# Performance work log

Measured on AMD Instinct MI355X. Metric: run time of the kernel, lower is better.

Reference implementation:

```python
import jax, jax.numpy as jnp
import numpy as np

N_HEAD_FULL = 16  # config.n_head

def setup_inputs() -> dict:
    key = jax.random.key(0)
    ks = jax.random.split(key, 5)
    B, T, D = 2, 2048, 2048
    s = 0.02
    return {
        "x": jax.random.normal(ks[0], (B, T, D), dtype=jnp.float32),
        "Wq": jax.random.normal(ks[1], (D, D), dtype=jnp.float32) * s,
        "Wk": jax.random.normal(ks[2], (D, D), dtype=jnp.float32) * s,
        "Wv": jax.random.normal(ks[3], (D, D), dtype=jnp.float32) * s,
        "Wo": jax.random.normal(ks[4], (D, D), dtype=jnp.float32) * s,
        "active_dim": 1024,
        "active_kv": 64,
    }

def reference(x, Wq, Wk, Wv, Wo, active_dim, active_kv):
    B, T, D = x.shape
    d = active_dim if active_dim is not None else D
    head_dim_base = D // N_HEAD_FULL          # 128
    kv_dim = active_kv if active_kv is not None else head_dim_base
    n_head = d // head_dim_base               # active heads
    head_dim = d // n_head                    # == head_dim_base

    xs = x[..., :d]                            # [B,T,d]
    # F.linear(x, W[:d,:d]) == x @ W[:d,:d].T
    q = jnp.einsum('btc,dc->btd', xs, Wq[:d, :d])
    k = jnp.einsum('btc,dc->btd', xs, Wk[:d, :d])
    v = jnp.einsum('btc,dc->btd', xs, Wv[:d, :d])

    def split_heads(t):  # [B,T,d] -> [B,h,T,hd]
        return t.reshape(B, T, n_head, head_dim).transpose(0, 2, 1, 3)
    q, k, v = split_heads(q), split_heads(k), split_heads(v)

    if kv_dim < head_dim:
        q, k, v = q[..., :kv_dim], k[..., :kv_dim], v[..., :kv_dim]

    scale = 1.0 / np.sqrt(kv_dim).astype(np.float32)
    attn = jnp.einsum('bhqd,bhkd->bhqk', q, k) * scale  # [B,h,T,T]
    causal = jnp.tril(jnp.ones((T, T), dtype=bool))
    attn = jnp.where(causal, attn, jnp.float32(-jnp.inf))
    attn = jax.nn.softmax(attn, axis=-1)
    out = jnp.einsum('bhqk,bhkd->bhqd', attn, v)        # [B,h,T,kv]

    if kv_dim < head_dim:
        out = jnp.pad(out, ((0, 0), (0, 0), (0, 0), (0, head_dim - kv_dim)))
    out = out.transpose(0, 2, 1, 3).reshape(B, T, d)
    out = jnp.einsum('btc,dc->btd', out, Wo[:d, :d])
    if d < D:
        out = jnp.pad(out, ((0, 0), (0, 0), (0, D - d)))
    return out
```

## Files before the change

kernel.cpp:

```cpp
#include <hip/hip_runtime.h>
#include <hip/hip_bf16.h>

typedef __attribute__((ext_vector_type(8))) short bf16x8;
typedef __attribute__((ext_vector_type(4))) float f32x4;

#define MFMA16(a,b,c) __builtin_amdgcn_mfma_f32_16x16x32_bf16((a),(b),(c),0,0,0)

static __device__ __forceinline__ unsigned short f2bf(float f) {
    unsigned int u = __builtin_bit_cast(unsigned int, f);
    u += 0x7fffu + ((u >> 16) & 1u);
    return (unsigned short)(u >> 16);
}

static __device__ __forceinline__ void g2l16(const unsigned short* g, unsigned short* l) {
    __builtin_amdgcn_global_load_lds(
        (const __attribute__((address_space(1))) unsigned int*)g,
        (__attribute__((address_space(3))) unsigned int*)l,
        16, 0, 0);
}

#define BT     4096
#define DFULL  2048
#define DACT   1024
#define DKV    64
#define NSEL   512
#define TSEQ   2048
#define PADR   72

__global__ __launch_bounds__(256) void prep_kernel(
    const float* __restrict__ x,  const float* __restrict__ Wq,
    const float* __restrict__ Wk, const float* __restrict__ Wv,
    const float* __restrict__ Wo,
    unsigned short* __restrict__ xb,  unsigned short* __restrict__ Wqb,
    unsigned short* __restrict__ Wkb, unsigned short* __restrict__ Wvb,
    unsigned short* __restrict__ Wob, float* __restrict__ out)
{
    const int NA = (BT * DACT) / 8;
    const int NB = (NSEL * DACT) / 8;
    const int NC = (DACT * NSEL) / 8;
    const int ND = (BT * DACT) / 8;
    const int TOT = NA + 3 * NB + NC + ND;
    for (int u = blockIdx.x * blockDim.x + threadIdx.x; u < TOT;
         u += gridDim.x * blockDim.x) {
        if (u < NA) {
            int e = u * 8; int row = e >> 10, col = e & 1023;
            const float* s = x + (size_t)row * DFULL + col;
            f32x4 v0 = *(const f32x4*)s, v1 = *(const f32x4*)(s + 4);
            bf16x8 o;
            #pragma unroll
            for (int j = 0; j < 4; ++j) { o[j] = (short)f2bf(v0[j]); o[4+j] = (short)f2bf(v1[j]); }
            *(bf16x8*)(xb + e) = o;
        } else if (u < NA + 3 * NB) {
            int t = u - NA; int mat = t / NB; int q = t % NB;
            int e = q * 8; int n = e >> 10, c = e & 1023;
            const float* W = (mat == 0) ? Wq : (mat == 1) ? Wk : Wv;
            unsigned short* Wb = (mat == 0) ? Wqb : (mat == 1) ? Wkb : Wvb;
            int wrow = (n >> 6) * 128 + (n & 63);
            const float* s = W + (size_t)wrow * DFULL + c;
            f32x4 v0 = *(const f32x4*)s, v1 = *(const f32x4*)(s + 4);
            bf16x8 o;
            #pragma unroll
            for (int j = 0; j < 4; ++j) { o[j] = (short)f2bf(v0[j]); o[4+j] = (short)f2bf(v1[j]); }
            *(bf16x8*)(Wb + e) = o;
        } else if (u < NA + 3 * NB + NC) {
            int q = u - NA - 3 * NB;
            int e = q * 8; int r = e >> 9, cs = e & 511;
            int col = (cs >> 6) * 128 + (cs & 63);
            const float* s = Wo + (size_t)r * DFULL + col;
            f32x4 v0 = *(const f32x4*)s, v1 = *(const f32x4*)(s + 4);
            bf16x8 o;
            #pragma unroll
            for (int j = 0; j < 4; ++j) { o[j] = (short)f2bf(v0[j]); o[4+j] = (short)f2bf(v1[j]); }
            *(bf16x8*)(Wob + e) = o;
        } else {
            int q = u - (NA + 3 * NB + NC);
            int e = q * 8; int row = e >> 10, col = e & 1023;
            float* dp = out + (size_t)row * DFULL + DACT + col;
            f32x4 z = {0.f, 0.f, 0.f, 0.f};
            *(f32x4*)dp = z; *(f32x4*)(dp + 4) = z;
        }
    }
}

__global__ __launch_bounds__(256) void qkv_gemm(
    const unsigned short* __restrict__ xb,
    const unsigned short* __restrict__ Wall,
    unsigned short* __restrict__ Qb, unsigned short* __restrict__ Kb,
    unsigned short* __restrict__ Vb)
{
    __shared__ unsigned short As[128 * 64];
    __shared__ unsigned short Bs[128 * 64];
    const int m0 = blockIdx.x * 128, n0 = blockIdx.y * 128;
    const int tid = threadIdx.x, w = tid >> 6, l = tid & 63;
    const int lr = l & 15, g = l >> 4, lk = g * 8;
    const int wr = w >> 1, wc = w & 1;
    const int srow = l >> 3, scol = (l & 7) * 8;

    f32x4 acc[4][4] = {};
    for (int k0 = 0; k0 < DACT; k0 += 64) {
        __syncthreads();
        #pragma unroll
        for (int i = 0; i < 4; ++i) {
            int chunk = w * 4 + i;
            int row = chunk * 8 + srow;
            g2l16(&xb[(size_t)(m0 + row) * DACT + k0 + scol], &As[chunk * 512]);
            g2l16(&Wall[(size_t)(n0 + row) * DACT + k0 + scol], &Bs[chunk * 512]);
        }
        __syncthreads();
        #pragma unroll
        for (int kk = 0; kk < 64; kk += 32) {
            bf16x8 a[4], b[4];
            #pragma unroll
            for (int m = 0; m < 4; ++m)
                a[m] = *(const bf16x8*)&As[(wr * 64 + m * 16 + lr) * 64 + kk + lk];
            #pragma unroll
            for (int n = 0; n < 4; ++n)
                b[n] = *(const bf16x8*)&Bs[(wc * 64 + n * 16 + lr) * 64 + kk + lk];
            #pragma unroll
            for (int m = 0; m < 4; ++m)
                #pragma unroll
                for (int n = 0; n < 4; ++n)
                    acc[m][n] = MFMA16(a[m], b[n], acc[m][n]);
        }
    }
    #pragma unroll
    for (int m = 0; m < 4; ++m)
        #pragma unroll
        for (int n = 0; n < 4; ++n)
            #pragma unroll
            for (int i = 0; i < 4; ++i) {
                int row = m0 + wr * 64 + m * 16 + g * 4 + i;
                int col = n0 + wc * 64 + n * 16 + lr;
                int mat = col >> 9, r = col & 511, h = r >> 6, j = r & 63;
                int bb = row >> 11, t = row & 2047, bh = bb * 8 + h;
                float v = acc[m][n][i];
                if (mat == 0)
                    Qb[((size_t)bh * TSEQ + t) * DKV + j] = f2bf(v * 0.125f);
                else if (mat == 1)
                    Kb[((size_t)bh * TSEQ + t) * DKV + (j ^ ((t & 7) << 3))] = f2bf(v);
                else
                    Vb[((size_t)bh * TSEQ + t) * DKV + j] = f2bf(v);
            }
}

__global__ __launch_bounds__(256) void vtrans_kernel(
    const unsigned short* __restrict__ Vb, unsigned short* __restrict__ Vtb)
{
    __shared__ unsigned short Ls[64 * PADR];
    const int t0 = blockIdx.x * 64, bh = blockIdx.y;
    const int tid = threadIdx.x;
    #pragma unroll
    for (int it = 0; it < 2; ++it) {
        int r = (tid >> 3) + it * 32, c = (tid & 7) * 8;
        *(bf16x8*)&Ls[r * PADR + c] =
            *(const bf16x8*)&Vb[((size_t)bh * TSEQ + t0 + r) * DKV + c];
    }
    __syncthreads();
    int dv = tid >> 2, tt0 = (tid & 3) * 16;
    unsigned short tmp[16];
    #pragma unroll
    for (int j = 0; j < 16; ++j) tmp[j] = Ls[(tt0 + j) * PADR + dv];
    const int sw = (dv & 7) << 3;
    size_t tb = (((size_t)bh * 32 + (t0 >> 6)) * 64 + dv) * 64;
    *(bf16x8*)&Vtb[tb + (tt0 ^ sw)]       = *(bf16x8*)&tmp[0];
    *(bf16x8*)&Vtb[tb + ((tt0 + 8) ^ sw)] = *(bf16x8*)&tmp[8];
}

__global__ __launch_bounds__(256) void attn_kernel(
    const unsigned short* __restrict__ Qb,
    const unsigned short* __restrict__ Kb,
    const unsigned short* __restrict__ Vtb,
    unsigned short* __restrict__ att)
{
    __shared__ unsigned short KV[2][2][4096];
    __shared__ unsigned short Ps[4][16 * PADR];
    const int f = blockIdx.x;
    const int bh = f & 15;
    const int S = 31 - (f >> 4);
    const int nt = S + 1;
    const int tid = threadIdx.x, w = tid >> 6, l = tid & 63;
    const int lr = l & 15, g = l >> 4, lk = g * 8;
    const size_t kvb = (size_t)bh * TSEQ * DKV;
    const int bb = bh >> 3, h = bh & 7;
    const int qs0 = S * 64 + w * 16;

    unsigned short* Psw = Ps[w];
    const short os = (short)0x3F80;
    const bf16x8 ones = {os, os, os, os, os, os, os, os};

    bf16x8 qf0 = *(const bf16x8*)&Qb[kvb + (size_t)(qs0 + lr) * DKV + lk];
    bf16x8 qf1 = *(const bf16x8*)&Qb[kvb + (size_t)(qs0 + lr) * DKV + 32 + lk];

    f32x4 acc[4] = {};
    f32x4 dacc = {};

    #define STAGE(b, jt)                                                      \
        do {                                                                  \
            const unsigned short* Ks_ = Kb + kvb + (size_t)(jt) * 4096 + w * 1024; \
            const unsigned short* Vs_ = Vtb + kvb + (size_t)(jt) * 4096 + w * 1024; \
            unsigned short* kd_ = &KV[b][0][w * 1024];                        \
            unsigned short* vd_ = &KV[b][1][w * 1024];                        \
            g2l16(&Ks_[l * 8], kd_);                                          \
            g2l16(&Ks_[512 + l * 8], kd_ + 512);                              \
            g2l16(&Vs_[l * 8], vd_);                                          \
            g2l16(&Vs_[512 + l * 8], vd_ + 512);                              \
        } while (0)

    STAGE(0, 0);
    __syncthreads();

    for (int jt = 0; jt < nt; ++jt) {
        const int cur = jt & 1;
        if (jt + 1 < nt) STAGE(cur ^ 1, jt + 1);

        const unsigned short* Kt = KV[cur][0];
        const unsigned short* Vt = KV[cur][1];

        #pragma unroll
        for (int c = 0; c < 4; ++c) {
            const int row = c * 16 + lr, sr = (row & 7) << 3;
            bf16x8 b0 = *(const bf16x8*)&Kt[row * 64 + (lk ^ sr)];
            bf16x8 b1 = *(const bf16x8*)&Kt[row * 64 + ((32 + lk) ^ sr)];
            f32x4 z = {};
            z = MFMA16(qf0, b0, z);
            z = MFMA16(qf1, b1, z);
            if (jt == nt - 1) {
                int kcol = jt * 64 + c * 16 + lr;
                #pragma unroll
                for (int i = 0; i < 4; ++i)
                    if (kcol > qs0 + g * 4 + i) z[i] = -64.f;
            }
            #pragma unroll
            for (int i = 0; i < 4; ++i)
                Psw[(g * 4 + i) * PADR + c * 16 + lr] = f2bf(__expf(z[i]));
        }
        bf16x8 pa0 = *(const bf16x8*)&Psw[lr * PADR + lk];
        bf16x8 pa1 = *(const bf16x8*)&Psw[lr * PADR + 32 + lk];

        #pragma unroll
        for (int n = 0; n < 4; ++n) {
            const int row = n * 16 + lr, sr = (row & 7) << 3;
            bf16x8 v0 = *(const bf16x8*)&Vt[row * 64 + (lk ^ sr)];
            bf16x8 v1 = *(const bf16x8*)&Vt[row * 64 + ((32 + lk) ^ sr)];
            acc[n] = MFMA16(pa0, v0, acc[n]);
            acc[n] = MFMA16(pa1, v1, acc[n]);
        }
        dacc = MFMA16(pa0, ones, dacc);
        dacc = MFMA16(pa1, ones, dacc);

        __syncthreads();
    }
    #undef STAGE

    #pragma unroll
    for (int i = 0; i < 4; ++i) {
        float inv = 1.0f / dacc[i];
        int t = qs0 + g * 4 + i;
        #pragma unroll
        for (int n = 0; n < 4; ++n)
            att[((size_t)bb * TSEQ + t) * NSEL + h * 64 + n * 16 + lr] =
                f2bf(acc[n][i] * inv);
    }
}

__global__ __launch_bounds__(256) void oproj_gemm(
    const unsigned short* __restrict__ att,
    const unsigned short* __restrict__ Wob,
    float* __restrict__ out)
{
    __shared__ unsigned short As[128 * 64];
    __shared__ unsigned short Bs[128 * 64];
    const int m0 = blockIdx.x * 128, n0 = blockIdx.y * 128;
    const int tid = threadIdx.x, w = tid >> 6, l = tid & 63;
    const int lr = l & 15, g = l >> 4, lk = g * 8;
    const int wr = w >> 1, wc = w & 1;
    const int srow = l >> 3, scol = (l & 7) * 8;

    f32x4 acc[4][4] = {};
    for (int k0 = 0; k0 < NSEL; k0 += 64) {
        __syncthreads();
        #pragma unroll
        for (int i = 0; i < 4; ++i) {
            int chunk = w * 4 + i;
            int row = chunk * 8 + srow;
            g2l16(&att[(size_t)(m0 + row) * NSEL + k0 + scol], &As[chunk * 512]);
            g2l16(&Wob[(size_t)(n0 + row) * NSEL + k0 + scol], &Bs[chunk * 512]);
        }
        __syncthreads();
        #pragma unroll
        for (int kk = 0; kk < 64; kk += 32) {
            bf16x8 a[4], b[4];
            #pragma unroll
            for (int m = 0; m < 4; ++m)
                a[m] = *(const bf16x8*)&As[(wr * 64 + m * 16 + lr) * 64 + kk + lk];
            #pragma unroll
            for (int n = 0; n < 4; ++n)
                b[n] = *(const bf16x8*)&Bs[(wc * 64 + n * 16 + lr) * 64 + kk + lk];
            #pragma unroll
            for (int m = 0; m < 4; ++m)
                #pragma unroll
                for (int n = 0; n < 4; ++n)
                    acc[m][n] = MFMA16(a[m], b[n], acc[m][n]);
        }
    }
    #pragma unroll
    for (int m = 0; m < 4; ++m)
        #pragma unroll
        for (int n = 0; n < 4; ++n)
            #pragma unroll
            for (int i = 0; i < 4; ++i) {
                int row = m0 + wr * 64 + m * 16 + g * 4 + i;
                int col = n0 + wc * 64 + n * 16 + lr;
                out[(size_t)row * DFULL + col] = acc[m][n][i];
            }
}

extern "C" void kernel_launch(void* const* d_in, const int* in_sizes, int n_in,
                              void* d_out, int out_size, void* d_ws, size_t ws_size,
                              hipStream_t stream) {
    const float* x  = (const float*)d_in[0];
    const float* Wq = (const float*)d_in[1];
    const float* Wk = (const float*)d_in[2];
    const float* Wv = (const float*)d_in[3];
    const float* Wo = (const float*)d_in[4];
    float* out = (float*)d_out;

    char* ws = (char*)d_ws;
    unsigned short* xb  = (unsigned short*)(ws);
    unsigned short* Wqb = (unsigned short*)(ws + 8388608);
    unsigned short* Wkb = (unsigned short*)(ws + 9437184);
    unsigned short* Wvb = (unsigned short*)(ws + 10485760);
    unsigned short* Wob = (unsigned short*)(ws + 11534336);
    unsigned short* Qb  = (unsigned short*)(ws + 12582912);
    unsigned short* Kb  = (unsigned short*)(ws + 16777216);
    unsigned short* Vtb = (unsigned short*)(ws + 20971520);
    unsigned short* Vb  = (unsigned short*)(ws + 25165824);
    unsigned short* att = (unsigned short*)(ws + 25165824);

    prep_kernel<<<2048, 256, 0, stream>>>(x, Wq, Wk, Wv, Wo,
                                          xb, Wqb, Wkb, Wvb, Wob, out);
    qkv_gemm<<<dim3(32, 12), 256, 0, stream>>>(xb, Wqb, Qb, Kb, Vb);
    vtrans_kernel<<<dim3(32, 16), 256, 0, stream>>>(Vb, Vtb);
    attn_kernel<<<512, 256, 0, stream>>>(Qb, Kb, Vtb, att);
    oproj_gemm<<<dim3(32, 8), 256, 0, stream>>>(att, Wob, out);
}
```

Measured before the change: 95.62 us.

## Split attention KV loop across wave pairs and halve QKV GEMM M-tile

The attention kernel now runs 512 threads per block. Each pair of waves shares a 16-row query slice and processes alternating KV tiles, so two tiles are staged per step. The partial numerators and denominators of the two waves are summed through shared memory at the end, and the P buffer uses an XOR swizzle instead of padding. The QKV GEMM switches to a 64x128 tile with a doubled grid for more blocks on the GPU. This trades extra LDS traffic, a reduction step and higher LDS use per block for more parallelism on the long causal rows.

```diff
diff --git a/kernel.cpp b/kernel.cpp
--- a/kernel.cpp
+++ b/kernel.cpp
@@ -88,48 +88,53 @@
     unsigned short* __restrict__ Qb, unsigned short* __restrict__ Kb,
     unsigned short* __restrict__ Vb)
 {
-    __shared__ unsigned short As[128 * 64];
+    __shared__ unsigned short As[64 * 64];
     __shared__ unsigned short Bs[128 * 64];
-    const int m0 = blockIdx.x * 128, n0 = blockIdx.y * 128;
+    const int m0 = blockIdx.x * 64, n0 = blockIdx.y * 128;
     const int tid = threadIdx.x, w = tid >> 6, l = tid & 63;
     const int lr = l & 15, g = l >> 4, lk = g * 8;
     const int wr = w >> 1, wc = w & 1;
     const int srow = l >> 3, scol = (l & 7) * 8;
 
-    f32x4 acc[4][4] = {};
+    f32x4 acc[2][4] = {};
     for (int k0 = 0; k0 < DACT; k0 += 64) {
         __syncthreads();
+        #pragma unroll
+        for (int i = 0; i < 2; ++i) {
+            int chunk = w * 2 + i;
+            int row = chunk * 8 + srow;
+            g2l16(&xb[(size_t)(m0 + row) * DACT + k0 + scol], &As[chunk * 512]);
+        }
         #pragma unroll
         for (int i = 0; i < 4; ++i) {
             int chunk = w * 4 + i;
             int row = chunk * 8 + srow;
-            g2l16(&xb[(size_t)(m0 + row) * DACT + k0 + scol], &As[chunk * 512]);
             g2l16(&Wall[(size_t)(n0 + row) * DACT + k0 + scol], &Bs[chunk * 512]);
         }
         __syncthreads();
         #pragma unroll
         for (int kk = 0; kk < 64; kk += 32) {
-            bf16x8 a[4], b[4];
-            #pragma unroll
-            for (int m = 0; m < 4; ++m)
-                a[m] = *(const bf16x8*)&As[(wr * 64 + m * 16 + lr) * 64 + kk + lk];
+            bf16x8 a[2], b[4];
+            #pragma unroll
+            for (int m = 0; m < 2; ++m)
+                a[m] = *(const bf16x8*)&As[(wr * 32 + m * 16 + lr) * 64 + kk + lk];
             #pragma unroll
             for (int n = 0; n < 4; ++n)
                 b[n] = *(const bf16x8*)&Bs[(wc * 64 + n * 16 + lr) * 64 + kk + lk];
             #pragma unroll
-            for (int m = 0; m < 4; ++m)
+            for (int m = 0; m < 2; ++m)
                 #pragma unroll
                 for (int n = 0; n < 4; ++n)
                     acc[m][n] = MFMA16(a[m], b[n], acc[m][n]);
         }
     }
     #pragma unroll
-    for (int m = 0; m < 4; ++m)
+    for (int m = 0; m < 2; ++m)
         #pragma unroll
         for (int n = 0; n < 4; ++n)
             #pragma unroll
             for (int i = 0; i < 4; ++i) {
-                int row = m0 + wr * 64 + m * 16 + g * 4 + i;
+                int row = m0 + wr * 32 + m * 16 + g * 4 + i;
                 int col = n0 + wc * 64 + n * 16 + lr;
                 int mat = col >> 9, r = col & 511, h = r >> 6, j = r & 63;
                 int bb = row >> 11, t = row & 2047, bh = bb * 8 + h;
@@ -166,23 +171,25 @@
     *(bf16x8*)&Vtb[tb + ((tt0 + 8) ^ sw)] = *(bf16x8*)&tmp[8];
 }
 
-__global__ __launch_bounds__(256) void attn_kernel(
+__global__ __launch_bounds__(512, 4) void attn_kernel(
     const unsigned short* __restrict__ Qb,
     const unsigned short* __restrict__ Kb,
     const unsigned short* __restrict__ Vtb,
     unsigned short* __restrict__ att)
 {
-    __shared__ unsigned short KV[2][2][4096];
-    __shared__ unsigned short Ps[4][16 * PADR];
+    __shared__ unsigned short KV[2][2][2][4096];
+    __shared__ unsigned short Ps[8][16 * 64];
     const int f = blockIdx.x;
     const int bh = f & 15;
     const int S = 31 - (f >> 4);
-    const int nt = S + 1;
+    const int ntt = S + 1;
+    const int np = (ntt + 1) >> 1;
     const int tid = threadIdx.x, w = tid >> 6, l = tid & 63;
     const int lr = l & 15, g = l >> 4, lk = g * 8;
+    const int s = w >> 1, j = w & 1;
     const size_t kvb = (size_t)bh * TSEQ * DKV;
     const int bb = bh >> 3, h = bh & 7;
-    const int qs0 = S * 64 + w * 16;
+    const int qs0 = S * 64 + s * 16;
 
     unsigned short* Psw = Ps[w];
     const short os = (short)0x3F80;
@@ -194,72 +201,100 @@
     f32x4 acc[4] = {};
     f32x4 dacc = {};
 
-    #define STAGE(b, jt)                                                      \
-        do {                                                                  \
-            const unsigned short* Ks_ = Kb + kvb + (size_t)(jt) * 4096 + w * 1024; \
-            const unsigned short* Vs_ = Vtb + kvb + (size_t)(jt) * 4096 + w * 1024; \
-            unsigned short* kd_ = &KV[b][0][w * 1024];                        \
-            unsigned short* vd_ = &KV[b][1][w * 1024];                        \
-            g2l16(&Ks_[l * 8], kd_);                                          \
-            g2l16(&Ks_[512 + l * 8], kd_ + 512);                              \
-            g2l16(&Vs_[l * 8], vd_);                                          \
-            g2l16(&Vs_[512 + l * 8], vd_ + 512);                              \
+    #define STAGE(b, p)                                                        \
+        do {                                                                   \
+            int r_ = w >> 1, par_ = r_ >> 1, kv_ = r_ & 1;                     \
+            int t_ = 2 * (p) + par_;                                           \
+            if (t_ < ntt) {                                                    \
+                const unsigned short* src_ =                                   \
+                    (kv_ ? Vtb : Kb) + kvb + (size_t)t_ * 4096 + (w & 1) * 2048; \
+                unsigned short* dst_ = &KV[b][par_][kv_][(w & 1) * 2048];      \
+                g2l16(&src_[l * 8],        dst_);                              \
+                g2l16(&src_[512 + l * 8],  dst_ + 512);                        \
+                g2l16(&src_[1024 + l * 8], dst_ + 1024);                       \
+                g2l16(&src_[1536 + l * 8], dst_ + 1536);                       \
+            }                                                                  \
         } while (0)
 
     STAGE(0, 0);
     __syncthreads();
 
-    for (int jt = 0; jt < nt; ++jt) {
-        const int cur = jt & 1;
-        if (jt + 1 < nt) STAGE(cur ^ 1, jt + 1);
-
-        const unsigned short* Kt = KV[cur][0];
-        const unsigned short* Vt = KV[cur][1];
-
-        #pragma unroll
-        for (int c = 0; c < 4; ++c) {
-            const int row = c * 16 + lr, sr = (row & 7) << 3;
-            bf16x8 b0 = *(const bf16x8*)&Kt[row * 64 + (lk ^ sr)];
-            bf16x8 b1 = *(const bf16x8*)&Kt[row * 64 + ((32 + lk) ^ sr)];
-            f32x4 z = {};
-            z = MFMA16(qf0, b0, z);
-            z = MFMA16(qf1, b1, z);
-            if (jt == nt - 1) {
-                int kcol = jt * 64 + c * 16 + lr;
+    for (int p = 0; p < np; ++p) {
+        const int cur = p & 1;
+        if (p + 1 < np) STAGE(cur ^ 1, p + 1);
+
+        const int jt = 2 * p + j;
+        if (jt < ntt) {
+            const unsigned short* Kt = KV[cur][j][0];
+            const unsigned short* Vt = KV[cur][j][1];
+
+            #pragma unroll
+            for (int c = 0; c < 4; ++c) {
+                const int row = c * 16 + lr, sr = (row & 7) << 3;
+                bf16x8 b0 = *(const bf16x8*)&Kt[row * 64 + (lk ^ sr)];
+                bf16x8 b1 = *(const bf16x8*)&Kt[row * 64 + ((32 + lk) ^ sr)];
+                f32x4 z = {};
+                z = MFMA16(qf0, b0, z);
+                z = MFMA16(qf1, b1, z);
+                if (jt == ntt - 1) {
+                    int kcol = jt * 64 + c * 16 + lr;
+                    #pragma unroll
+                    for (int i = 0; i < 4; ++i)
+                        if (kcol > qs0 + g * 4 + i) z[i] = -64.f;
+                }
                 #pragma unroll
-                for (int i = 0; i < 4; ++i)
-                    if (kcol > qs0 + g * 4 + i) z[i] = -64.f;
-            }
+                for (int i = 0; i < 4; ++i) {
+                    const int prow = g * 4 + i;
+                    Psw[prow * 64 + ((c * 16 + lr) ^ ((prow & 7) << 3))] =
+                        f2bf(__expf(z[i]));
+                }
+            }
+            const int psr = (lr & 7) << 3;
+            bf16x8 pa0 = *(const bf16x8*)&Psw[lr * 64 + (lk ^ psr)];
+            bf16x8 pa1 = *(const bf16x8*)&Psw[lr * 64 + ((32 + lk) ^ psr)];
+
+            #pragma unroll
+            for (int n = 0; n < 4; ++n) {
+                const int row = n * 16 + lr, sr = (row & 7) << 3;
+                bf16x8 v0 = *(const bf16x8*)&Vt[row * 64 + (lk ^ sr)];
+                bf16x8 v1 = *(const bf16x8*)&Vt[row * 64 + ((32 + lk) ^ sr)];
+                acc[n] = MFMA16(pa0, v0, acc[n]);
+                acc[n] = MFMA16(pa1, v1, acc[n]);
+            }
+            dacc = MFMA16(pa0, ones, dacc);
+            dacc = MFMA16(pa1, ones, dacc);
+        }
+        __syncthreads();
+    }
+    #undef STAGE
+
+    float* M = (float*)KV;
+    if (j == 1) {
+        #pragma unroll
+        for (int n = 0; n < 4; ++n)
             #pragma unroll
             for (int i = 0; i < 4; ++i)
-                Psw[(g * 4 + i) * PADR + c * 16 + lr] = f2bf(__expf(z[i]));
-        }
-        bf16x8 pa0 = *(const bf16x8*)&Psw[lr * PADR + lk];
-        bf16x8 pa1 = *(const bf16x8*)&Psw[lr * PADR + 32 + lk];
-
-        #pragma unroll
-        for (int n = 0; n < 4; ++n) {
-            const int row = n * 16 + lr, sr = (row & 7) << 3;
-            bf16x8 v0 = *(const bf16x8*)&Vt[row * 64 + (lk ^ sr)];
-            bf16x8 v1 = *(const bf16x8*)&Vt[row * 64 + ((32 + lk) ^ sr)];
-            acc[n] = MFMA16(pa0, v0, acc[n]);
-            acc[n] = MFMA16(pa1, v1, acc[n]);
-        }
-        dacc = MFMA16(pa0, ones, dacc);
-        dacc = MFMA16(pa1, ones, dacc);
-
-        __syncthreads();
-    }
-    #undef STAGE
-
-    #pragma unroll
-    for (int i = 0; i < 4; ++i) {
-        float inv = 1.0f / dacc[i];
-        int t = qs0 + g * 4 + i;
-        #pragma unroll
-        for (int n = 0; n < 4; ++n)
-            att[((size_t)bb * TSEQ + t) * NSEL + h * 64 + n * 16 + lr] =
-                f2bf(acc[n][i] * inv);
+                M[s * 1088 + (g * 4 + i) * 64 + n * 16 + lr] = acc[n][i];
+        if (lr == 0) {
+            #pragma unroll
+            for (int i = 0; i < 4; ++i)
+                M[s * 1088 + 1024 + g * 4 + i] = dacc[i];
+        }
+    }
+    __syncthreads();
+    if (j == 0) {
+        #pragma unroll
+        for (int i = 0; i < 4; ++i) {
+            float den = dacc[i] + M[s * 1088 + 1024 + g * 4 + i];
+            float inv = 1.0f / den;
+            int t = qs0 + g * 4 + i;
+            #pragma unroll
+            for (int n = 0; n < 4; ++n) {
+                float v = acc[n][i] + M[s * 1088 + (g * 4 + i) * 64 + n * 16 + lr];
+                att[((size_t)bb * TSEQ + t) * NSEL + h * 64 + n * 16 + lr] =
+                    f2bf(v * inv);
+            }
+        }
     }
 }
 
@@ -339,8 +374,8 @@
 
     prep_kernel<<<2048, 256, 0, stream>>>(x, Wq, Wk, Wv, Wo,
                                           xb, Wqb, Wkb, Wvb, Wob, out);
-    qkv_gemm<<<dim3(32, 12), 256, 0, stream>>>(xb, Wqb, Qb, Kb, Vb);
+    qkv_gemm<<<dim3(64, 12), 256, 0, stream>>>(xb, Wqb, Qb, Kb, Vb);
     vtrans_kernel<<<dim3(32, 16), 256, 0, stream>>>(Vb, Vtb);
-    attn_kernel<<<512, 256, 0, stream>>>(Qb, Kb, Vtb, att);
+    attn_kernel<<<512, 512, 0, stream>>>(Qb, Kb, Vtb, att);
     oproj_gemm<<<dim3(32, 8), 256, 0, stream>>>(att, Wob, out);
 }
```

Measured after the change: 83.58 us. 12.6% less time.
